# Performance work log

Measured on AMD Instinct MI355X. Metric: run time of the kernel, lower is better.

## Reference

```python
import jax, jax.numpy as jnp
import numpy as np

ORDER = 2  # gcn_order (max diffusion step)


def _diffusion_conv(x, supports, W, b):
    """DCRNN diffusion graph conv.
    x: (B, C, N); supports: list of (N, N); W: (C*(len(supports)*ORDER+1), O); b: (O,)
    Chebyshev-style recurrence x_k = 2*A@x_{k-1} - x_{k-2}, as in original DCRNN.
    """
    feats = [x]
    for A in supports:
        x0 = x
        x1 = jnp.einsum('bcn,mn->bcm', x0, A)
        feats.append(x1)
        for _ in range(2, ORDER + 1):
            x2 = 2.0 * jnp.einsum('bcn,mn->bcm', x1, A) - x0
            feats.append(x2)
            x0, x1 = x1, x2
    h = jnp.concatenate(feats, axis=1)  # (B, C*num_matrices, N)
    return jnp.einsum('bcn,co->bon', h, W) + b[None, :, None]


def setup_inputs() -> dict:
    key = jax.random.key(0)
    ks = jax.random.split(key, 8)
    B, IN_DIM, HID, N = 64, 2, 64, 2048
    NUM_MAT = 2 * ORDER + 1  # num_supports*order + 1
    CIN = IN_DIM + HID  # 66
    inputs = jax.random.normal(ks[0], (B, IN_DIM, N), dtype=jnp.float32)
    hx = jax.random.normal(ks[1], (B, HID, N), dtype=jnp.float32)
    # random-walk style supports: nonnegative, row-normalized
    a0 = jax.random.uniform(ks[2], (N, N), dtype=jnp.float32)
    a1 = jax.random.uniform(ks[3], (N, N), dtype=jnp.float32)
    support0 = a0 / jnp.sum(a0, axis=1, keepdims=True)
    support1 = a1 / jnp.sum(a1, axis=1, keepdims=True)
    scale = 1.0 / np.sqrt(CIN * NUM_MAT)
    W_ru = jax.random.normal(ks[4], (CIN * NUM_MAT, 2 * HID), dtype=jnp.float32) * scale
    b_ru = jnp.ones((2 * HID,), dtype=jnp.float32)  # bias_start = 1.0
    W_c = jax.random.normal(ks[5], (CIN * NUM_MAT, HID), dtype=jnp.float32) * scale
    b_c = jnp.zeros((HID,), dtype=jnp.float32)
    return {"inputs": inputs, "hx": hx, "support0": support0, "support1": support1,
            "W_ru": W_ru, "b_ru": b_ru, "W_c": W_c, "b_c": b_c}


def reference(inputs, hx, support0, support1, W_ru, b_ru, W_c, b_c):
    supports = [support0, support1]
    hid = hx.shape[1]
    concat_input = jnp.concatenate([inputs, hx], axis=1)  # (B, in+hid, N)
    value = jax.nn.sigmoid(_diffusion_conv(concat_input, supports, W_ru, b_ru))
    r = value[:, :hid, :]
    u = value[:, hid:, :]
    C = jnp.tanh(_diffusion_conv(jnp.concatenate([inputs, r * hx], axis=1), supports, W_c, b_c))
    new_state = u * hx + (1.0 - u) * C
    return new_state
```

## Files before the change

### kernel.cpp

```cpp
#include <hip/hip_runtime.h>
#include <stdint.h>


typedef unsigned short ushort_t;
typedef __attribute__((ext_vector_type(8))) __bf16 bf16x8;
typedef __attribute__((ext_vector_type(4))) float f32x4;
typedef __attribute__((ext_vector_type(16))) float f32x16;
typedef __attribute__((ext_vector_type(8))) int i32x8;

#define KP 352
#define MROWS 131072

__device__ __forceinline__ ushort_t f2bf(float f) {
  union { float f; uint32_t u; } v; v.f = f;
  uint32_t r = v.u + 0x7FFFu + ((v.u >> 16) & 1u);
  return (ushort_t)(r >> 16);
}
__device__ __forceinline__ float bf2f(ushort_t u) {
  union { uint32_t u; float f; } v; v.u = ((uint32_t)u) << 16;
  return v.f;
}

__device__ __forceinline__ void gl_lds16(const void* g, void* l) {
  __builtin_amdgcn_global_load_lds(
      (const __attribute__((address_space(1))) void*)g,
      (__attribute__((address_space(3))) void*)l, 16, 0, 0);
}


__global__ void k_cast_f8(const float* __restrict__ src, uint32_t* __restrict__ dst,
                          int n4, float scale) {
  for (int i = blockIdx.x * 256 + threadIdx.x; i < n4; i += gridDim.x * 256) {
    float4 v = ((const float4*)src)[i];
    int r = __builtin_amdgcn_cvt_pk_fp8_f32(v.x * scale, v.y * scale, 0, 0);
    r = __builtin_amdgcn_cvt_pk_fp8_f32(v.z * scale, v.w * scale, r, 1);
    dst[i] = (uint32_t)r;
  }
}

__global__ void k_build_X(const float* __restrict__ inputs, const float* __restrict__ hx,
                          ushort_t* __restrict__ Xbf, uint8_t* __restrict__ Xf8) {
  int r = blockIdx.x;
  int b = r / 66, c = r - b * 66;
  const float* src = (c < 2) ? (inputs + ((size_t)b * 2 + c) * 2048)
                             : (hx + ((size_t)b * 64 + (c - 2)) * 2048);
  ushort_t* d1 = Xbf + (size_t)r * 2048;
  uint8_t* d2 = Xf8 + (size_t)r * 2048;
  for (int n = threadIdx.x * 4; n < 2048; n += 256 * 4) {
    float4 v = *(const float4*)(src + n);
    ushort4 rr;
    rr.x = f2bf(v.x); rr.y = f2bf(v.y); rr.z = f2bf(v.z); rr.w = f2bf(v.w);
    *(ushort4*)(d1 + n) = rr;
    int r8 = __builtin_amdgcn_cvt_pk_fp8_f32(v.x, v.y, 0, 0);
    r8 = __builtin_amdgcn_cvt_pk_fp8_f32(v.z, v.w, r8, 1);
    *(uint32_t*)(d2 + n) = (uint32_t)r8;
  }
}

__global__ void k_pack_W(const float* __restrict__ W, int O, ushort_t* __restrict__ Wt) {
  int o = blockIdx.x;
  for (int k = threadIdx.x; k < KP; k += 256) {
    float v = (k < 330 && o < O) ? W[(size_t)k * O + o] : 0.f;
    Wt[(size_t)o * KP + k] = f2bf(v);
  }
}

__global__ __launch_bounds__(256) void k_trans_slot0(const ushort_t* __restrict__ Xbf,
                                                     ushort_t* __restrict__ Ht) {
  __shared__ ushort_t t[66 * 136];
  const int tid = threadIdx.x;
  const int b = blockIdx.y;
  const int n0 = blockIdx.x * 128;
  for (int idx = tid; idx < 66 * 16; idx += 256) {
    int c = idx >> 4, seg = idx & 15;
    bf16x8 v = *(const bf16x8*)&Xbf[((size_t)b * 66 + c) * 2048 + n0 + seg * 8];
    *(bf16x8*)&t[c * 136 + seg * 8] = v;
  }
  __syncthreads();
  for (int idx = tid; idx < 128 * 66; idx += 256) {
    int nn = idx / 66, c = idx - nn * 66;
    Ht[((size_t)b * 2048 + n0 + nn) * KP + c] = t[c * 136 + nn];
  }
}

template <int MODE>
__global__ __launch_bounds__(256, 4) void gemm_bt(
    const uint8_t* __restrict__ Aop, int lda,
    const uint8_t* __restrict__ Bop,
    const ushort_t* __restrict__ Xres,
    uint8_t* __restrict__ Y1f8,
    ushort_t* __restrict__ Ht) {
  __shared__ char smem[33280];
  ushort_t* smemU = (ushort_t*)smem;
  const int tid = threadIdx.x;
  const int l = tid & 63, w = tid >> 6;
  const int wr = w >> 1, wc = w & 1;
  const int rowL = l & 31;
  const int kh = l >> 5;
  const int m7 = (rowL >> 2) & 7;

  const int fid = blockIdx.y * 33 + blockIdx.x;
  const int xcd = fid & 7;
  const int idx = fid >> 3;
  const int nb = xcd * 4 + idx / 33;
  const int mb = idx % 33;
  const int r0 = mb * 128;
  const int m0 = nb * 128;
  const int g = m0 >> 11;
  if (MODE == 1) Aop += (size_t)g * 2048;

  const int SA = (MODE == 0) ? 0x7F7F7F7F : 0x7A7A7A7A;
  const int SB = 0x76767676;

  f32x16 acc[2][2];
#pragma unroll
  for (int mi = 0; mi < 2; ++mi)
#pragma unroll
    for (int ni = 0; ni < 2; ++ni)
#pragma unroll
      for (int q = 0; q < 16; ++q) acc[mi][ni][q] = 0.f;

  {
  }
  const int d = tid;
  const int srow = ((d >> 3) << 2) | (((d >> 1) ^ (d >> 4)) & 1) |
                   ((((d >> 2) ^ (d >> 5)) & 1) << 1);
  const int sj = (d ^ (d >> 3)) & 1;
  const uint8_t* pA = Aop + (size_t)(r0 + srow) * lda + sj * 16;
  const uint8_t* pB = Bop + (size_t)(m0 + srow) * 2048 + sj * 16;

  const int sj0 = ((rowL * 2) ^ m7) * 16;
  const int sj1 = ((rowL * 2 + 1) ^ m7) * 16;
  const int aw = wr * 2048;
  const int bw = wc * 2048;

  for (int kt = 0; kt < 16; ++kt) {
    const int kb = kt * 128;
#pragma unroll
    for (int kq = 0; kq < 4; ++kq) {
      gl_lds16(pA + kb + kq * 32, smem + kq * 4096 + tid * 16);
      gl_lds16(pB + kb + kq * 32, smem + 16384 + kq * 4096 + tid * 16);
    }
    __syncthreads();
#pragma unroll
    for (int kw = 0; kw < 2; ++kw) {
      const int rbase = (2 * kw + kh) * 4096;
      union { uint4 q[2]; i32x8 v; } bu[2], au;
#pragma unroll
      for (int ni = 0; ni < 2; ++ni) {
        const char* bp = smem + 16384 + rbase + bw + ni * 1024;
        bu[ni].q[0] = *(const uint4*)(bp + sj0);
        bu[ni].q[1] = *(const uint4*)(bp + sj1);
      }
#pragma unroll
      for (int mi = 0; mi < 2; ++mi) {
        const char* ap = smem + rbase + aw + mi * 1024;
        au.q[0] = *(const uint4*)(ap + sj0);
        au.q[1] = *(const uint4*)(ap + sj1);
#pragma unroll
        for (int ni = 0; ni < 2; ++ni)
          acc[mi][ni] = __builtin_amdgcn_mfma_scale_f32_32x32x64_f8f6f4(
              au.v, bu[ni].v, acc[mi][ni], 0, 0, 0, SA, 0, SB);
      }
    }
    __syncthreads();
  }

#pragma unroll
  for (int mi = 0; mi < 2; ++mi) {
#pragma unroll
    for (int ni = 0; ni < 2; ++ni) {
      const int clb = wc * 64 + ni * 32 + rowL;
#pragma unroll
      for (int q = 0; q < 16; ++q) {
        const int rl = wr * 64 + mi * 32 + (q & 3) + 8 * (q >> 2) + 4 * kh;
        float v = acc[mi][ni][q];
        if (MODE == 1)
          v = 2.f * v - bf2f(Xres[(size_t)(r0 + rl) * 2048 + ((m0 + clb) & 2047)]);
        smemU[clb * 130 + rl] = f2bf(v);
      }
    }
  }
  __syncthreads();

  const int slotBase = (MODE == 0 ? 1 : 2) + 2 * g;
  const int n_base = m0 & 2047;
#pragma unroll 4
  for (int j2 = 0; j2 < 64; ++j2) {
    int idx2 = j2 * 256 + tid;
    int mc = idx2 >> 7, rl = idx2 & 127;
    unsigned rg = (unsigned)(r0 + rl);
    unsigned b = rg / 66u;
    unsigned c = rg - b * 66u;
    int n = n_base + mc;
    Ht[((size_t)b * 2048 + n) * KP + slotBase * 66 + c] = smemU[mc * 130 + rl];
  }

  if (MODE == 0) {
#pragma unroll 4
    for (int it = 0; it < 16; ++it) {
      int idx2 = it * 256 + tid;
      int rl = idx2 >> 5, mq = idx2 & 31;
      float v0 = bf2f(smemU[(mq * 4 + 0) * 130 + rl]) * 32.f;
      float v1 = bf2f(smemU[(mq * 4 + 1) * 130 + rl]) * 32.f;
      float v2 = bf2f(smemU[(mq * 4 + 2) * 130 + rl]) * 32.f;
      float v3 = bf2f(smemU[(mq * 4 + 3) * 130 + rl]) * 32.f;
      int r8 = __builtin_amdgcn_cvt_pk_fp8_f32(v0, v1, 0, 0);
      r8 = __builtin_amdgcn_cvt_pk_fp8_f32(v2, v3, r8, 1);
      *(uint32_t*)(Y1f8 + (size_t)(r0 + rl) * 4096 + m0 + mq * 4) = (uint32_t)r8;
    }
  }
}

template <int MODE>
__global__ __launch_bounds__(256, 4) void proj_mfma(
    const ushort_t* __restrict__ Ht, const ushort_t* __restrict__ Wt,
    const float* __restrict__ bias, const float* __restrict__ hx,
    ushort_t* __restrict__ Xbf, uint8_t* __restrict__ Xf8,
    ushort_t* __restrict__ Ubuf, float* __restrict__ out) {
  __shared__ ushort_t smem[16640];
  const int tid = threadIdx.x;
  const int l = tid & 63, w = tid >> 6;
  const int wr = w >> 1, wc = w & 1;
  const int lr = l & 15, lk = l >> 4;
  const int bb = blockIdx.x >> 4;
  const int n0 = (blockIdx.x & 15) * 128;
  const size_t m0 = (size_t)bb * 2048 + n0;

  f32x4 acc[4][4];
  const f32x4 zero = {0.f, 0.f, 0.f, 0.f};
#pragma unroll
  for (int mi = 0; mi < 4; mi++)
#pragma unroll
    for (int ni = 0; ni < 4; ni++) acc[mi][ni] = zero;

  const int srow = tid >> 2;
  const int kcol = ((tid & 3) ^ ((tid >> 3) & 3)) * 8;
  const ushort_t* pA = Ht + (m0 + srow) * KP + kcol;
  const ushort_t* pB = Wt + (size_t)srow * KP + kcol;
  const int so = (lk ^ ((lr >> 1) & 3)) * 8;

#define STAGEP(KT, BB)                                                         \
  {                                                                            \
    const int kp_ = (KT) * 32;                                                 \
    gl_lds16(pA + kp_, (void*)&smem[(BB) + tid * 8]);                          \
    gl_lds16(pA + (size_t)64 * KP + kp_, (void*)&smem[(BB) + 2048 + tid * 8]); \
    gl_lds16(pB + kp_, (void*)&smem[(BB) + 4096 + tid * 8]);                   \
    gl_lds16(pB + (size_t)64 * KP + kp_, (void*)&smem[(BB) + 6144 + tid * 8]); \
  }

#define COMPUTEP(BB)                                                           \
  {                                                                            \
    bf16x8 af[4], bfv[4];                                                      \
    _Pragma("unroll")                                                          \
    for (int i = 0; i < 4; i++)                                                \
      af[i] = *(const bf16x8*)&smem[(BB) + (wr * 64 + i * 16 + lr) * 32 + so]; \
    _Pragma("unroll")                                                          \
    for (int i = 0; i < 4; i++)                                                \
      bfv[i] = *(const bf16x8*)&smem[(BB) + 4096 + (wc * 64 + i * 16 + lr) * 32 + so]; \
    _Pragma("unroll")                                                          \
    for (int mi = 0; mi < 4; mi++)                                             \
      _Pragma("unroll")                                                        \
      for (int ni = 0; ni < 4; ni++)                                           \
        acc[mi][ni] = __builtin_amdgcn_mfma_f32_16x16x32_bf16(af[mi], bfv[ni], \
                                                              acc[mi][ni], 0, 0, 0); \
  }

  STAGEP(0, 0);
  __syncthreads();
#pragma unroll 1
  for (int kt = 0; kt < 11; ++kt) {
    if (kt + 1 < 11) STAGEP(kt + 1, ((kt + 1) & 1) * 8192);
    COMPUTEP((kt & 1) * 8192);
    __syncthreads();
  }

#undef STAGEP
#undef COMPUTEP

#pragma unroll
  for (int mi = 0; mi < 4; mi++) {
#pragma unroll
    for (int ni = 0; ni < 4; ni++) {
      const int rl0 = wr * 64 + mi * 16 + lk * 4;
      const int o = wc * 64 + ni * 16 + lr;
      float bv = (MODE == 0 || o < 64) ? bias[o] : 0.f;
#pragma unroll
      for (int j = 0; j < 4; j++) {
        float v = acc[mi][ni][j] + bv;
        float s;
        if (MODE == 0) s = 1.f / (1.f + expf(-v));
        else           s = tanhf(v);
        smem[o * 130 + rl0 + j] = f2bf(s);
      }
    }
  }
  __syncthreads();

  if (MODE == 0) {
#pragma unroll 4
    for (int j2 = 0; j2 < 64; ++j2) {
      int idx = j2 * 256 + tid;
      int o = idx >> 7, m = idx & 127;
      ushort_t sv = smem[o * 130 + m];
      int n = n0 + m;
      if (o < 64) {
        float s = bf2f(sv);
        float hxv = hx[((size_t)bb * 64 + o) * 2048 + n];
        float p = s * hxv;
        Xbf[((size_t)bb * 66 + 2 + o) * 2048 + n] = f2bf(p);
        int r8 = __builtin_amdgcn_cvt_pk_fp8_f32(p, 0.f, 0, 0);
        Xf8[((size_t)bb * 66 + 2 + o) * 2048 + n] = (uint8_t)(r8 & 0xFF);
      } else {
        Ubuf[((size_t)bb * 64 + (o - 64)) * 2048 + n] = sv;
      }
    }
  } else {
#pragma unroll 4
    for (int j2 = 0; j2 < 32; ++j2) {
      int idx = j2 * 256 + tid;
      int o = idx >> 7, m = idx & 127;
      float Cv = bf2f(smem[o * 130 + m]);
      int n = n0 + m;
      size_t oi = ((size_t)bb * 64 + o) * 2048 + n;
      float u = bf2f(Ubuf[oi]);
      out[oi] = u * hx[oi] + (1.f - u) * Cv;
    }
  }
}


extern "C" void kernel_launch(void* const* d_in, const int* in_sizes, int n_in,
                              void* d_out, int out_size, void* d_ws, size_t ws_size,
                              hipStream_t stream) {
  (void)in_sizes; (void)n_in; (void)out_size; (void)ws_size;
  const float* inputs = (const float*)d_in[0];
  const float* hx     = (const float*)d_in[1];
  const float* s0     = (const float*)d_in[2];
  const float* s1     = (const float*)d_in[3];
  const float* W_ru   = (const float*)d_in[4];
  const float* b_ru   = (const float*)d_in[5];
  const float* W_c    = (const float*)d_in[6];
  const float* b_c    = (const float*)d_in[7];
  float* out = (float*)d_out;

  char* p = (char*)d_ws;
  uint8_t*  Abf8 = (uint8_t*)p;  p += (size_t)4096 * 2048;
  ushort_t* Xbf  = (ushort_t*)p; p += (size_t)4224 * 2048 * 2;
  uint8_t*  Xf8  = (uint8_t*)p;  p += (size_t)4224 * 2048;
  uint8_t*  Y1f8 = (uint8_t*)p;  p += (size_t)4224 * 4096;
  ushort_t* Ht   = (ushort_t*)p; p += (size_t)MROWS * KP * 2;
  ushort_t* Ubuf = (ushort_t*)p; p += (size_t)64 * 64 * 2048 * 2;
  ushort_t* Wtru = (ushort_t*)p; p += (size_t)128 * KP * 2;
  ushort_t* Wtc  = (ushort_t*)p; p += (size_t)128 * KP * 2;

  k_cast_f8<<<1024, 256, 0, stream>>>(s0, (uint32_t*)Abf8, 1048576, 512.f);
  k_cast_f8<<<1024, 256, 0, stream>>>(s1, (uint32_t*)(Abf8 + 4194304), 1048576, 512.f);
  k_build_X<<<4224, 256, 0, stream>>>(inputs, hx, Xbf, Xf8);
  k_pack_W<<<128, 256, 0, stream>>>(W_ru, 128, Wtru);
  k_pack_W<<<128, 256, 0, stream>>>(W_c, 64, Wtc);

  dim3 g(33, 32);
  dim3 gt(16, 64);
  k_trans_slot0<<<gt, 256, 0, stream>>>(Xbf, Ht);
  gemm_bt<0><<<g, 256, 0, stream>>>(Xf8, 2048, Abf8, nullptr, Y1f8, Ht);
  gemm_bt<1><<<g, 256, 0, stream>>>(Y1f8, 4096, Abf8, Xbf, nullptr, Ht);
  proj_mfma<0><<<1024, 256, 0, stream>>>(Ht, Wtru, b_ru, hx, Xbf, Xf8, Ubuf, nullptr);
  k_trans_slot0<<<gt, 256, 0, stream>>>(Xbf, Ht);
  gemm_bt<0><<<g, 256, 0, stream>>>(Xf8, 2048, Abf8, nullptr, Y1f8, Ht);
  gemm_bt<1><<<g, 256, 0, stream>>>(Y1f8, 4096, Abf8, Xbf, nullptr, Ht);
  proj_mfma<1><<<1024, 256, 0, stream>>>(Ht, Wtc, b_c, hx, nullptr, nullptr, Ubuf, out);
}
```

Before: 470.4 us.

## Fuse slot-0 transpose into gate projection and pack narrow Ht stores

The r*hx product is now staged in shared memory inside the first projection kernel, then written to Xbf/Xf8 with vectorized stores and transposed directly into Ht slot 0. This removes the second k_trans_slot0 launch and its re-read of Xbf. Ht scatter stores in the transpose and GEMM epilogues are packed into 32-bit writes, and the two W pack launches are merged into one. The GEMM K loop start is rotated per block, presumably to spread memory-channel traffic. Columns 0-1 of slot 0 (the inputs) are not rewritten, which is correct because they are unchanged from the first pass. One extra barrier is added to the projection epilogue.

```diff
diff --git a/kernel.cpp b/kernel.cpp
--- a/kernel.cpp
+++ b/kernel.cpp
@@ -57,11 +57,16 @@
   }
 }
 
-__global__ void k_pack_W(const float* __restrict__ W, int O, ushort_t* __restrict__ Wt) {
+__global__ void k_pack_W(const float* __restrict__ Wru, const float* __restrict__ Wc,
+                         ushort_t* __restrict__ Wtru, ushort_t* __restrict__ Wtc) {
   int o = blockIdx.x;
+  const float* W = (o < 128) ? Wru : Wc;
+  int O = (o < 128) ? 128 : 64;
+  int oo = (o < 128) ? o : (o - 128);
+  ushort_t* Wt = (o < 128) ? Wtru : Wtc;
   for (int k = threadIdx.x; k < KP; k += 256) {
-    float v = (k < 330 && o < O) ? W[(size_t)k * O + o] : 0.f;
-    Wt[(size_t)o * KP + k] = f2bf(v);
+    float v = (k < 330 && oo < O) ? W[(size_t)k * O + oo] : 0.f;
+    Wt[(size_t)oo * KP + k] = f2bf(v);
   }
 }
 
@@ -77,9 +82,11 @@
     *(bf16x8*)&t[c * 136 + seg * 8] = v;
   }
   __syncthreads();
-  for (int idx = tid; idx < 128 * 66; idx += 256) {
-    int nn = idx / 66, c = idx - nn * 66;
-    Ht[((size_t)b * 2048 + n0 + nn) * KP + c] = t[c * 136 + nn];
+  for (int idx = tid; idx < 128 * 33; idx += 256) {
+    int nn = idx / 33, pc = idx - nn * 33;
+    int c = pc * 2;
+    uint32_t pk = (uint32_t)t[c * 136 + nn] | ((uint32_t)t[(c + 1) * 136 + nn] << 16);
+    *(uint32_t*)&Ht[((size_t)b * 2048 + n0 + nn) * KP + c] = pk;
   }
 }
 
@@ -120,8 +127,6 @@
 #pragma unroll
       for (int q = 0; q < 16; ++q) acc[mi][ni][q] = 0.f;
 
-  {
-  }
   const int d = tid;
   const int srow = ((d >> 3) << 2) | (((d >> 1) ^ (d >> 4)) & 1) |
                    ((((d >> 2) ^ (d >> 5)) & 1) << 1);
@@ -134,7 +139,9 @@
   const int aw = wr * 2048;
   const int bw = wc * 2048;
 
-  for (int kt = 0; kt < 16; ++kt) {
+  const int kt0 = (idx & 3) * 4;
+  for (int ktt = 0; ktt < 16; ++ktt) {
+    const int kt = (ktt + kt0) & 15;
     const int kb = kt * 128;
 #pragma unroll
     for (int kq = 0; kq < 4; ++kq) {
@@ -186,14 +193,17 @@
   const int slotBase = (MODE == 0 ? 1 : 2) + 2 * g;
   const int n_base = m0 & 2047;
 #pragma unroll 4
-  for (int j2 = 0; j2 < 64; ++j2) {
+  for (int j2 = 0; j2 < 32; ++j2) {
     int idx2 = j2 * 256 + tid;
-    int mc = idx2 >> 7, rl = idx2 & 127;
+    int mc = idx2 >> 6, pr = idx2 & 63;
+    int rl = pr * 2;
     unsigned rg = (unsigned)(r0 + rl);
     unsigned b = rg / 66u;
     unsigned c = rg - b * 66u;
     int n = n_base + mc;
-    Ht[((size_t)b * 2048 + n) * KP + slotBase * 66 + c] = smemU[mc * 130 + rl];
+    uint32_t pk = (uint32_t)smemU[mc * 130 + rl] |
+                  ((uint32_t)smemU[mc * 130 + rl + 1] << 16);
+    *(uint32_t*)&Ht[((size_t)b * 2048 + n) * KP + slotBase * 66 + c] = pk;
   }
 
   if (MODE == 0) {
@@ -214,10 +224,11 @@
 
 template <int MODE>
 __global__ __launch_bounds__(256, 4) void proj_mfma(
-    const ushort_t* __restrict__ Ht, const ushort_t* __restrict__ Wt,
+    const ushort_t* __restrict__ Ht_c, const ushort_t* __restrict__ Wt,
     const float* __restrict__ bias, const float* __restrict__ hx,
     ushort_t* __restrict__ Xbf, uint8_t* __restrict__ Xf8,
-    ushort_t* __restrict__ Ubuf, float* __restrict__ out) {
+    ushort_t* __restrict__ Ubuf, ushort_t* __restrict__ HtW,
+    float* __restrict__ out) {
   __shared__ ushort_t smem[16640];
   const int tid = threadIdx.x;
   const int l = tid & 63, w = tid >> 6;
@@ -236,7 +247,7 @@
 
   const int srow = tid >> 2;
   const int kcol = ((tid & 3) ^ ((tid >> 3) & 3)) * 8;
-  const ushort_t* pA = Ht + (m0 + srow) * KP + kcol;
+  const ushort_t* pA = Ht_c + (m0 + srow) * KP + kcol;
   const ushort_t* pB = Wt + (size_t)srow * KP + kcol;
   const int so = (lk ^ ((lr >> 1) & 3)) * 8;
 
@@ -303,17 +314,34 @@
       int idx = j2 * 256 + tid;
       int o = idx >> 7, m = idx & 127;
       ushort_t sv = smem[o * 130 + m];
-      int n = n0 + m;
       if (o < 64) {
-        float s = bf2f(sv);
-        float hxv = hx[((size_t)bb * 64 + o) * 2048 + n];
-        float p = s * hxv;
-        Xbf[((size_t)bb * 66 + 2 + o) * 2048 + n] = f2bf(p);
-        int r8 = __builtin_amdgcn_cvt_pk_fp8_f32(p, 0.f, 0, 0);
-        Xf8[((size_t)bb * 66 + 2 + o) * 2048 + n] = (uint8_t)(r8 & 0xFF);
+        float p = bf2f(sv) * hx[((size_t)bb * 64 + o) * 2048 + n0 + m];
+        smem[o * 130 + m] = f2bf(p);
       } else {
-        Ubuf[((size_t)bb * 64 + (o - 64)) * 2048 + n] = sv;
-      }
+        Ubuf[((size_t)bb * 64 + (o - 64)) * 2048 + n0 + m] = sv;
+      }
+    }
+    __syncthreads();
+#pragma unroll 2
+    for (int j2 = 0; j2 < 8; ++j2) {
+      int idx = j2 * 256 + tid;
+      int o = idx >> 5, m4 = (idx & 31) * 4;
+      ushort_t s0 = smem[o * 130 + m4 + 0], s1 = smem[o * 130 + m4 + 1];
+      ushort_t s2 = smem[o * 130 + m4 + 2], s3 = smem[o * 130 + m4 + 3];
+      ushort4 pk4; pk4.x = s0; pk4.y = s1; pk4.z = s2; pk4.w = s3;
+      *(ushort4*)&Xbf[((size_t)bb * 66 + 2 + o) * 2048 + n0 + m4] = pk4;
+      int r8 = __builtin_amdgcn_cvt_pk_fp8_f32(bf2f(s0), bf2f(s1), 0, 0);
+      r8 = __builtin_amdgcn_cvt_pk_fp8_f32(bf2f(s2), bf2f(s3), r8, 1);
+      *(uint32_t*)(Xf8 + ((size_t)bb * 66 + 2 + o) * 2048 + n0 + m4) = (uint32_t)r8;
+    }
+#pragma unroll 2
+    for (int j2 = 0; j2 < 16; ++j2) {
+      int idx = j2 * 256 + tid;
+      int m = idx >> 5, po = idx & 31;
+      int o = po * 2;
+      uint32_t pk = (uint32_t)smem[o * 130 + m] |
+                    ((uint32_t)smem[(o + 1) * 130 + m] << 16);
+      *(uint32_t*)&HtW[((size_t)bb * 2048 + n0 + m) * KP + 2 + o] = pk;
     }
   } else {
 #pragma unroll 4
@@ -357,17 +385,15 @@
   k_cast_f8<<<1024, 256, 0, stream>>>(s0, (uint32_t*)Abf8, 1048576, 512.f);
   k_cast_f8<<<1024, 256, 0, stream>>>(s1, (uint32_t*)(Abf8 + 4194304), 1048576, 512.f);
   k_build_X<<<4224, 256, 0, stream>>>(inputs, hx, Xbf, Xf8);
-  k_pack_W<<<128, 256, 0, stream>>>(W_ru, 128, Wtru);
-  k_pack_W<<<128, 256, 0, stream>>>(W_c, 64, Wtc);
+  k_pack_W<<<192, 256, 0, stream>>>(W_ru, W_c, Wtru, Wtc);
 
   dim3 g(33, 32);
   dim3 gt(16, 64);
   k_trans_slot0<<<gt, 256, 0, stream>>>(Xbf, Ht);
   gemm_bt<0><<<g, 256, 0, stream>>>(Xf8, 2048, Abf8, nullptr, Y1f8, Ht);
   gemm_bt<1><<<g, 256, 0, stream>>>(Y1f8, 4096, Abf8, Xbf, nullptr, Ht);
-  proj_mfma<0><<<1024, 256, 0, stream>>>(Ht, Wtru, b_ru, hx, Xbf, Xf8, Ubuf, nullptr);
-  k_trans_slot0<<<gt, 256, 0, stream>>>(Xbf, Ht);
+  proj_mfma<0><<<1024, 256, 0, stream>>>(Ht, Wtru, b_ru, hx, Xbf, Xf8, Ubuf, Ht, nullptr);
   gemm_bt<0><<<g, 256, 0, stream>>>(Xf8, 2048, Abf8, nullptr, Y1f8, Ht);
   gemm_bt<1><<<g, 256, 0, stream>>>(Y1f8, 4096, Abf8, Xbf, nullptr, Ht);
-  proj_mfma<1><<<1024, 256, 0, stream>>>(Ht, Wtc, b_c, hx, nullptr, nullptr, Ubuf, out);
-}
+  proj_mfma<1><<<1024, 256, 0, stream>>>(Ht, Wtc, b_c, hx, nullptr, nullptr, Ubuf, nullptr, out);
+}
```

After: 446.6 us. 1.05x faster.
